# Kernel tuning notes

Hardware: AMD Instinct MI355X
Metric: run time of the kernel (lower is better)

## Reference

```python
import jax, jax.numpy as jnp
import numpy as np

K = 3
KK = K * K


def conv3x3(x, w, b):
    # x: [B,C,H,W], w: [O,C,3,3]
    y = jax.lax.conv_general_dilated(x, w, (1, 1), ((1, 1), (1, 1)),
                                     dimension_numbers=('NCHW', 'OIHW', 'NCHW'))
    return y + b[None, :, None, None]


def deform_conv(x, offset, w, b):
    # torchvision.ops.deform_conv2d, 3x3, pad=1, stride=1, no mask.
    B, C, H, W = x.shape
    off = offset.reshape(B, KK, 2, H, W)  # per kernel tap: (dy, dx)
    ky = jnp.repeat(jnp.arange(K, dtype=x.dtype) - 1, K)  # [9]
    kx = jnp.tile(jnp.arange(K, dtype=x.dtype) - 1, K)
    py = jnp.arange(H, dtype=x.dtype)[None, None, :, None] + ky[None, :, None, None] + off[:, :, 0]
    px = jnp.arange(W, dtype=x.dtype)[None, None, None, :] + kx[None, :, None, None] + off[:, :, 1]
    y0 = jnp.floor(py)
    x0 = jnp.floor(px)
    wy = (py - y0)[:, None]  # [B,1,9,H,W]
    wx = (px - x0)[:, None]
    y0i = y0.astype(jnp.int32)
    x0i = x0.astype(jnp.int32)
    xf = x.reshape(B, C, H * W)

    def corner(yi, xi):
        valid = ((yi >= 0) & (yi < H) & (xi >= 0) & (xi < W))
        idx = jnp.clip(yi, 0, H - 1) * W + jnp.clip(xi, 0, W - 1)  # [B,9,H,W]
        g = jax.vmap(lambda xb, ib: xb[:, ib.reshape(-1)])(xf, idx)  # [B,C,9*H*W]
        return g.reshape(B, C, KK, H, W) * valid[:, None].astype(x.dtype)

    val = (corner(y0i, x0i) * (1 - wy) * (1 - wx)
           + corner(y0i, x0i + 1) * (1 - wy) * wx
           + corner(y0i + 1, x0i) * wy * (1 - wx)
           + corner(y0i + 1, x0i + 1) * wy * wx)  # [B,C,9,H,W]
    out = jnp.einsum('bckhw,ock->bohw', val, w.reshape(w.shape[0], C, KK))
    return out + b[None, :, None, None]


def se_gate(x, w1, b1, w2, b2):
    # global avg pool -> 1x1 conv -> relu -> 1x1 conv -> sigmoid -> scale
    m = x.mean((2, 3))  # [B,C]
    h = jax.nn.relu(jnp.einsum('bc,rc->br', m, w1) + b1)
    g = jax.nn.sigmoid(jnp.einsum('br,cr->bc', h, w2) + b2)
    return x * g[:, :, None, None]


def resize_bilinear(x, oh, ow):
    # F.interpolate(mode='bilinear', align_corners=False)
    B, C, H, W = x.shape

    def coords(n_in, n_out):
        src = (jnp.arange(n_out, dtype=x.dtype) + 0.5) * (n_in / n_out) - 0.5
        src = jnp.clip(src, 0.0, n_in - 1)
        i0 = jnp.floor(src).astype(jnp.int32)
        i1 = jnp.minimum(i0 + 1, n_in - 1)
        return i0, i1, (src - i0).astype(x.dtype)

    y0, y1, wy = coords(H, oh)
    x = x[:, :, y0, :] * (1 - wy)[None, None, :, None] + x[:, :, y1, :] * wy[None, None, :, None]
    c0, c1, wc = coords(W, ow)
    x = x[:, :, :, c0] * (1 - wc)[None, None, None, :] + x[:, :, :, c1] * wc[None, None, None, :]
    return x


def setup_inputs() -> dict:
    key = jax.random.key(0)
    ks = jax.random.split(key, 12)
    B, C, H, W = 4, 64, 128, 128
    L, O, R = 4, 64, 4  # levels, out_channels, reduction=64//16
    d = {
        'x': jax.random.normal(ks[0], (B, C, H, W), jnp.float32),
        'off_w': jax.random.normal(ks[1], (L, 2 * KK, C, 3, 3), jnp.float32) * 0.01,
        'off_b': jax.random.normal(ks[2], (L, 2 * KK), jnp.float32) * 0.01,
        'dc_w': jax.random.normal(ks[3], (L, O, C, 3, 3), jnp.float32) * 0.05,
        'dc_b': jax.random.normal(ks[4], (L, O), jnp.float32) * 0.05,
        'se_w1': jax.random.normal(ks[5], (L, R, O), jnp.float32) * 0.1,
        'se_b1': jax.random.normal(ks[6], (L, R), jnp.float32) * 0.1,
        'se_w2': jax.random.normal(ks[7], (L, O, R), jnp.float32) * 0.1,
        'se_b2': jax.random.normal(ks[8], (L, O), jnp.float32) * 0.1,
        'fuse_w': jax.random.normal(ks[9], (O, L * O), jnp.float32) * 0.05,
        'fuse_b': jax.random.normal(ks[10], (O,), jnp.float32) * 0.05,
    }
    return d


def reference(x, off_w, off_b, dc_w, dc_b, se_w1, se_b1, se_w2, se_b2, fuse_w, fuse_b):
    B, _, H, W = x.shape
    L = off_w.shape[0]
    cur = x
    feats = []
    for i in range(L):
        if i > 0:
            cur = resize_bilinear(cur, cur.shape[2] // 2, cur.shape[3] // 2)
        off = conv3x3(cur, off_w[i], off_b[i])
        cur = deform_conv(cur, off, dc_w[i], dc_b[i])
        cur = se_gate(cur, se_w1[i], se_b1[i], se_w2[i], se_b2[i])
        feats.append(resize_bilinear(cur, H, W))
    for i in range(L - 2, -1, -1):
        feats[i] = feats[i] + feats[i + 1]
    fused = jnp.concatenate(feats, axis=1)  # [B, L*O, H, W]
    return jnp.einsum('bchw,oc->bohw', fused, fuse_w) + fuse_b[None, :, None, None]
```

## Files before the change

### kernel.cpp

```cpp
#include <hip/hip_runtime.h>
#include <hip/hip_bf16.h>
#include <math.h>


constexpr int Bn = 4;

typedef __attribute__((ext_vector_type(8))) short short8;
typedef __attribute__((ext_vector_type(4))) float f32x4;
typedef __attribute__((ext_vector_type(4))) unsigned uint4v;

static __device__ __forceinline__ short f2b(float f){
  union { float f; unsigned u; } v; v.f = f;
  unsigned r = v.u + 0x7fffu + ((v.u >> 16) & 1u);
  return (short)(r >> 16);
}
static __device__ __forceinline__ unsigned f2b2(float x, float y){
  union { __hip_bfloat162 h; unsigned u; } cv;
  cv.h = __float22bfloat162_rn(make_float2(x, y));
  return cv.u;
}
static __device__ __forceinline__ float blo(unsigned u){ return __uint_as_float(u << 16); }
static __device__ __forceinline__ float bhi(unsigned u){ return __uint_as_float(u & 0xffff0000u); }

constexpr size_t OFF_CUR   = 0;
constexpr size_t OFF_DC    = OFF_CUR  + 4194304;
constexpr size_t OFF_T0    = OFF_DC   + 4194304;
constexpr size_t OFF_T1    = OFF_T0   + 4194304;
constexpr size_t OFF_T2    = OFF_T1   + 1048576;
constexpr size_t OFF_T3    = OFF_T2   + 262144;
constexpr size_t OFF_WSUMT = OFF_T3   + 65536;
constexpr size_t OFF_DCWT  = OFF_WSUMT + 8192;
constexpr size_t OFF_OWT   = OFF_DCWT  + 73728;
constexpr size_t OFF_SUMS  = OFF_OWT   + 36864;

__global__ void prep_k(const float* __restrict__ dc_w, const float* __restrict__ off_w,
                       const float* __restrict__ fuse_w, float* __restrict__ ws){
  int i = blockIdx.x * 256 + threadIdx.x;
  short* dcwT  = (short*)(ws + OFF_DCWT);
  short* owT   = (short*)(ws + OFF_OWT);
  short* wsumT = (short*)(ws + OFF_WSUMT);
  if (i < 147456){
    int oc = i / 576, r = i % 576, k = r >> 6, c = r & 63;
    dcwT[i] = f2b(dc_w[(oc*64 + c)*9 + k]);
  } else if (i < 147456 + 73728){
    int t = i - 147456;
    int lm = t / 576, l = lm >> 5, m = lm & 31, r = t % 576, k = r >> 6, c = r & 63;
    owT[t] = (m < 18) ? f2b(off_w[((l*18 + m)*64 + c)*9 + k]) : (short)0;
  } else if (i < 147456 + 73728 + 16384){
    int t = i - (147456 + 73728);
    int l = t / 4096, r = t % 4096, o = r / 64, c = r % 64;
    float s = 0.f;
    for (int jl = 0; jl <= l; jl++) s += fuse_w[o*256 + jl*64 + c];
    wsumT[t] = f2b(s);
  } else if (i < 147456 + 73728 + 16384 + 65536){
    ws[OFF_SUMS + (i - (147456 + 73728 + 16384))] = 0.f;
  }
}

__global__ __launch_bounds__(256) void cvt_k(const float* __restrict__ x, unsigned* __restrict__ cur){
  __shared__ float t[64][65];
  int tile = blockIdx.x;
  int b = tile >> 8, p0 = (tile & 255) << 6;
  int tx = threadIdx.x & 63, ty = threadIdx.x >> 6;
  #pragma unroll
  for (int c = ty; c < 64; c += 4)
    t[c][tx] = x[(((size_t)(b << 6) + c) << 14) + p0 + tx];
  __syncthreads();
  int u = threadIdx.x & 31, pr = threadIdx.x >> 5;
  #pragma unroll
  for (int i = 0; i < 8; i++){
    int pp = pr + i*8;
    unsigned v = f2b2(t[2*u][pp], t[2*u + 1][pp]);
    cur[((size_t)(b << 14) + p0 + pp)*32 + u] = v;
  }
}

template<int H, int LVL>
__global__ __launch_bounds__(256, 6) void deform_k(
    const unsigned* __restrict__ cur, const float* __restrict__ ws_all,
    const float* __restrict__ off_bias, const float* __restrict__ dc_bias,
    float* __restrict__ dc, float* __restrict__ sums){
  constexpr int W = H, P = H * W;
  constexpr int PITCHB = 584 * 2;
  constexpr int TPR = W/4, TPB = P/16;
  __shared__ __align__(16) short valA[16][584];
  __shared__ float offsP[2][16][18];
  __shared__ float4 tapW[144];
  __shared__ int4   tapI[144];
  const short* owt = (const short*)(ws_all + OFF_OWT) + LVL * 32 * 576;
  const short* dcw = (const short*)(ws_all + OFF_DCWT) + (size_t)LVL * 64 * 576;
  const int tid = threadIdx.x;
  const int wave = tid >> 6, lane = tid & 63;
  const int c0 = lane & 15, quad = lane >> 4, q4 = quad * 4;
  const int half = lane >> 5, cc = lane & 31;
  const int b = blockIdx.x / TPB;
  const int rr = blockIdx.x % TPB;
  const int hrow = (rr / TPR) * 4, wcol = (rr % TPR) * 4;
  const char* curc = (const char*)(cur + (size_t)b * P * 32) + cc * 4;
  char* valc = (char*)valA + wave * (4 * PITCHB);

  #pragma unroll
  for (int i = 0; i < 18; i++){
    const int t0 = 2*i, t1 = t0 + 1;
    const int p0l = t0/9, k0 = t0%9, p1l = t1/9, k1 = t1%9;
    int yy0 = hrow + wave + k0/3 - 1, xx0 = wcol + p0l + k0%3 - 1;
    int yy1 = hrow + wave + k1/3 - 1, xx1 = wcol + p1l + k1%3 - 1;
    bool v0 = ((unsigned)yy0 < (unsigned)H) & ((unsigned)xx0 < (unsigned)W);
    bool v1 = ((unsigned)yy1 < (unsigned)H) & ((unsigned)xx1 < (unsigned)W);
    int  i0 = v0 ? (yy0*W + xx0) : 0,  i1 = v1 ? (yy1*W + xx1) : 0;
    int   idx = half ? i1 : i0;
    bool  vv  = half ? v1 : v0;
    unsigned uv = *(const unsigned*)(curc + (size_t)idx * 128);
    uv = vv ? uv : 0u;
    const int ob0 = p0l*PITCHB + k0*128, ob1 = p1l*PITCHB + k1*128;
    *(unsigned*)(valc + (half ? ob1 : ob0) + cc*4) = uv;
  }
  __syncthreads();

  {
    const int colw = wave & 1, kh = wave >> 1;
    f32x4 oacc = {0,0,0,0};
    #pragma unroll
    for (int kb = 0; kb < 9; kb++){
      int kk = kh*9 + kb;
      short8 a  = *(const short8*)&valA[c0][kk*32 + quad*8];
      short8 bf = *(const short8*)&owt[(colw*16 + c0)*576 + kk*32 + quad*8];
      oacc = __builtin_amdgcn_mfma_f32_16x16x32_bf16(a, bf, oacc, 0, 0, 0);
    }
    int comp = colw*16 + c0;
    if (comp < 18){
      #pragma unroll
      for (int r = 0; r < 4; r++) offsP[kh][q4 + r][comp] = oacc[r];
    }
  }
  __syncthreads();

  if (tid < 144){
    int p = tid / 9, k = tid % 9;
    int h = hrow + (p >> 2), w = wcol + (p & 3);
    float oy = offsP[0][p][2*k]     + offsP[1][p][2*k]     + off_bias[LVL*18 + 2*k];
    float ox = offsP[0][p][2*k + 1] + offsP[1][p][2*k + 1] + off_bias[LVL*18 + 2*k + 1];
    float py = (float)(h + k/3 - 1) + oy;
    float px = (float)(w + k%3 - 1) + ox;
    float y0f = floorf(py), x0f = floorf(px);
    float fy = py - y0f, fx = px - x0f;
    int y0 = (int)y0f, x0 = (int)x0f, y1 = y0 + 1, x1 = x0 + 1;
    bool vy0 = (y0 >= 0) & (y0 < H), vy1 = (y1 >= 0) & (y1 < H);
    bool vx0 = (x0 >= 0) & (x0 < W), vx1 = (x1 >= 0) & (x1 < W);
    int y0c = min(max(y0, 0), H-1), y1c = min(max(y1, 0), H-1);
    int x0c = min(max(x0, 0), W-1), x1c = min(max(x1, 0), W-1);
    float gy = 1.f - fy, gx = 1.f - fx;
    tapW[tid] = make_float4((vy0 & vx0) ? gy*gx : 0.f,
                            (vy0 & vx1) ? gy*fx : 0.f,
                            (vy1 & vx0) ? fy*gx : 0.f,
                            (vy1 & vx1) ? fy*fx : 0.f);
    tapI[tid] = make_int4((y0c*W + x0c) << 7, (y0c*W + x1c) << 7,
                          (y1c*W + x0c) << 7, (y1c*W + x1c) << 7);
  }
  __syncthreads();

  #pragma unroll
  for (int i = 0; i < 18; i++){
    int T = wave*36 + 2*i + half;
    float4 wv = tapW[T];
    int4   ti = tapI[T];
    unsigned u0 = *(const unsigned*)(curc + ti.x);
    unsigned u1 = *(const unsigned*)(curc + ti.y);
    unsigned u2 = *(const unsigned*)(curc + ti.z);
    unsigned u3 = *(const unsigned*)(curc + ti.w);
    float vx = wv.x*blo(u0) + wv.y*blo(u1) + wv.z*blo(u2) + wv.w*blo(u3);
    float vy = wv.x*bhi(u0) + wv.y*bhi(u1) + wv.z*bhi(u2) + wv.w*bhi(u3);
    unsigned pk = f2b2(vx, vy);
    const int t0 = 2*i, t1 = t0 + 1;
    const int ob0 = (t0/9)*PITCHB + (t0%9)*128, ob1 = (t1/9)*PITCHB + (t1%9)*128;
    *(unsigned*)(valc + (half ? ob1 : ob0) + cc*4) = pk;
  }
  __syncthreads();

  const int n = wave*16 + c0;
  float bt2 = dc_bias[LVL*64 + n];
  f32x4 d0 = {bt2, bt2, bt2, bt2}, d1 = {0,0,0,0};
  #pragma unroll
  for (int kb = 0; kb < 9; kb++){
    short8 a  = *(const short8*)&valA[c0][kb*32 + quad*8];
    short8 bf = *(const short8*)&dcw[n*576 + kb*32 + quad*8];
    d0 = __builtin_amdgcn_mfma_f32_16x16x32_bf16(a, bf, d0, 0, 0, 0);
  }
  #pragma unroll
  for (int kb = 9; kb < 18; kb++){
    short8 a  = *(const short8*)&valA[c0][kb*32 + quad*8];
    short8 bf = *(const short8*)&dcw[n*576 + kb*32 + quad*8];
    d1 = __builtin_amdgcn_mfma_f32_16x16x32_bf16(a, bf, d1, 0, 0, 0);
  }
  f32x4 acc;
  #pragma unroll
  for (int r = 0; r < 4; r++) acc[r] = d0[r] + d1[r];
  float* dcb = dc + ((size_t)b*P + (size_t)(hrow + quad)*W + wcol)*64;
  #pragma unroll
  for (int r = 0; r < 4; r++) dcb[r*64 + n] = acc[r];
  float s = acc[0] + acc[1] + acc[2] + acc[3];
  s += __shfl_xor(s, 16);
  s += __shfl_xor(s, 32);
  if (quad == 0) atomicAdd(&sums[(LVL*16 + (blockIdx.x & 15))*256 + (b << 6) + n], s);
}

template<int W, int LVL>
__global__ __launch_bounds__(256) void fuse_gd_k(
    const float* __restrict__ dcv, const float* __restrict__ sums,
    const float* __restrict__ se_w1, const float* __restrict__ se_b1,
    const float* __restrict__ se_w2, const float* __restrict__ se_b2,
    const float* __restrict__ ws_all, float* __restrict__ tmp, unsigned* __restrict__ curn){
  constexpr int P = W * W;
  constexpr bool POOL = (LVL < 3);
  constexpr float invP = 1.f / (float)P;
  __shared__ __align__(16) float fS[64][68];
  __shared__ __align__(16) float gsh[64];
  const short* wsl = (const short*)(ws_all + OFF_WSUMT) + LVL * 4096;
  const int tid = threadIdx.x, wave = tid >> 6, lane = tid & 63;
  const int c0 = lane & 15, quad = lane >> 4, q4 = quad * 4;
  int b, rp = 0, cs = 0;
  if (POOL){
    constexpr int tilesPerB = P / 64, tilesPerRow = W / 32;
    b = blockIdx.x / tilesPerB;
    int r = blockIdx.x % tilesPerB;
    rp = r / tilesPerRow; cs = r % tilesPerRow;
  } else {
    b = (blockIdx.x * 64) / P;
  }

  {
    int sg = tid >> 6, c = tid & 63;
    float part = 0.f;
    #pragma unroll
    for (int s = 0; s < 4; s++) part += sums[(LVL*16 + sg*4 + s)*256 + (b << 6) + c];
    fS[sg][c] = part;
    __syncthreads();
    if (tid < 64){
      int r = tid & 3, j = tid >> 2;
      float hp = 0.f;
      #pragma unroll
      for (int q = 0; q < 4; q++){
        int cq = j*4 + q;
        float m = (fS[0][cq] + fS[1][cq] + fS[2][cq] + fS[3][cq]) * invP;
        hp += m * se_w1[(LVL*4 + r)*64 + cq];
      }
      hp += __shfl_xor(hp, 4);  hp += __shfl_xor(hp, 8);
      hp += __shfl_xor(hp, 16); hp += __shfl_xor(hp, 32);
      float hr = fmaxf(hp + se_b1[LVL*4 + r], 0.f);
      float a = se_b2[LVL*64 + tid];
      #pragma unroll
      for (int r2 = 0; r2 < 4; r2++)
        a += __shfl(hr, r2) * se_w2[(LVL*64 + tid)*4 + r2];
      gsh[tid] = 1.f / (1.f + expf(-a));
    }
    __syncthreads();
  }

  float4 g4 = *(const float4*)&gsh[c0*4];
  #pragma unroll
  for (int i = 0; i < 4; i++){
    int lp = wave*16 + (lane >> 4) + i*4;
    size_t gpix = POOL ? ((size_t)b*P + (size_t)(2*rp + (lp >> 5))*W + cs*32 + (lp & 31))
                       : ((size_t)blockIdx.x*64 + lp);
    float4 d = *(const float4*)&dcv[gpix*64 + c0*4];
    float4 v = make_float4(d.x*g4.x, d.y*g4.y, d.z*g4.z, d.w*g4.w);
    *(float4*)&fS[lp][c0*4] = v;
  }
  __syncthreads();
  f32x4 acc[4] = {{0,0,0,0},{0,0,0,0},{0,0,0,0},{0,0,0,0}};
  #pragma unroll
  for (int kb = 0; kb < 2; kb++){
    float4 lo = *(const float4*)&fS[wave*16 + c0][kb*32 + quad*8];
    float4 hi = *(const float4*)&fS[wave*16 + c0][kb*32 + quad*8 + 4];
    uint4v ua = {f2b2(lo.x, lo.y), f2b2(lo.z, lo.w), f2b2(hi.x, hi.y), f2b2(hi.z, hi.w)};
    short8 a = __builtin_bit_cast(short8, ua);
    #pragma unroll
    for (int t = 0; t < 4; t++){
      short8 bf = *(const short8*)&wsl[(t*16 + c0)*64 + kb*32 + quad*8];
      acc[t] = __builtin_amdgcn_mfma_f32_16x16x32_bf16(a, bf, acc[t], 0, 0, 0);
    }
  }
  #pragma unroll
  for (int t = 0; t < 4; t++){
    int n = t*16 + c0;
    size_t plane = ((size_t)(b << 6) + n) * P;
    size_t pix = POOL ? ((size_t)(2*rp + (wave >> 1))*W + cs*32 + (wave & 1)*16 + q4)
                      : ((size_t)(blockIdx.x*64) - (size_t)b*P + wave*16 + q4);
    *(f32x4*)&tmp[plane + pix] = acc[t];
  }
  if constexpr (POOL){
    int j = tid >> 4, uu = tid & 15;
    float4 p0 = *(const float4*)&fS[2*j][uu*4];
    float4 p1 = *(const float4*)&fS[2*j + 1][uu*4];
    float4 p2 = *(const float4*)&fS[32 + 2*j][uu*4];
    float4 p3 = *(const float4*)&fS[33 + 2*j][uu*4];
    float4 av = make_float4(0.25f*(p0.x + p1.x + p2.x + p3.x),
                            0.25f*(p0.y + p1.y + p2.y + p3.y),
                            0.25f*(p0.z + p1.z + p2.z + p3.z),
                            0.25f*(p0.w + p1.w + p2.w + p3.w));
    uint2 pv = make_uint2(f2b2(av.x, av.y), f2b2(av.z, av.w));
    *(uint2*)&curn[((size_t)b*(P/4) + (size_t)rp*(W/2) + cs*16 + j)*32 + uu*2] = pv;
  }
}

__global__ void final_k(const float* __restrict__ ws_all, const float* __restrict__ fuse_bias,
                        float* __restrict__ out){
  int i = blockIdx.x * 256 + threadIdx.x;
  int w = i & 127, h = (i >> 7) & 127, o = (i >> 14) & 63, b = i >> 20;
  float acc = fuse_bias[o] + ws_all[OFF_T0 + (((size_t)(b << 6) + o) << 14) + (h << 7) + w];
  const float* tarr[3] = {ws_all + OFF_T1, ws_all + OFF_T2, ws_all + OFF_T3};
  #pragma unroll
  for (int li = 0; li < 3; li++){
    int l = li + 1, Hl = 128 >> l;
    float scale = 1.0f / (float)(1 << l);
    float sy = fminf(fmaxf((h + 0.5f)*scale - 0.5f, 0.f), (float)(Hl - 1));
    float sx = fminf(fmaxf((w + 0.5f)*scale - 0.5f, 0.f), (float)(Hl - 1));
    int y0 = (int)sy, x0 = (int)sx;
    float fy = sy - y0, fx = sx - x0;
    int y1 = min(y0 + 1, Hl - 1), x1 = min(x0 + 1, Hl - 1);
    const float* tb = tarr[li] + (size_t)((b << 6) + o) * Hl * Hl;
    float v00 = tb[y0*Hl + x0], v01 = tb[y0*Hl + x1];
    float v10 = tb[y1*Hl + x0], v11 = tb[y1*Hl + x1];
    acc += (1.f-fy)*((1.f-fx)*v00 + fx*v01) + fy*((1.f-fx)*v10 + fx*v11);
  }
  out[i] = acc;
}

extern "C" void kernel_launch(void* const* d_in, const int* in_sizes, int n_in,
                              void* d_out, int out_size, void* d_ws, size_t ws_size,
                              hipStream_t stream){
  (void)in_sizes; (void)n_in; (void)out_size; (void)ws_size;
  const float* x      = (const float*)d_in[0];
  const float* off_w  = (const float*)d_in[1];
  const float* off_b  = (const float*)d_in[2];
  const float* dc_w   = (const float*)d_in[3];
  const float* dc_b   = (const float*)d_in[4];
  const float* se_w1  = (const float*)d_in[5];
  const float* se_b1  = (const float*)d_in[6];
  const float* se_w2  = (const float*)d_in[7];
  const float* se_b2  = (const float*)d_in[8];
  const float* fuse_w = (const float*)d_in[9];
  const float* fuse_b = (const float*)d_in[10];
  float* out = (float*)d_out;
  float* ws = (float*)d_ws;
  unsigned* cur = (unsigned*)(ws + OFF_CUR);
  float* dc   = ws + OFF_DC;
  float* tmp[4] = {ws + OFF_T0, ws + OFF_T1, ws + OFF_T2, ws + OFF_T3};
  float* sums = ws + OFF_SUMS;

  prep_k<<<(303104 + 255)/256, 256, 0, stream>>>(dc_w, off_w, fuse_w, ws);
  cvt_k<<<1024, 256, 0, stream>>>(x, cur);

  deform_k<128,0><<<4096, 256, 0, stream>>>(cur, ws, off_b, dc_b, dc, sums);
  fuse_gd_k<128,0><<<1024, 256, 0, stream>>>(dc, sums, se_w1, se_b1, se_w2, se_b2, ws, tmp[0], cur);
  deform_k<64,1><<<1024, 256, 0, stream>>>(cur, ws, off_b, dc_b, dc, sums);
  fuse_gd_k<64,1><<<256, 256, 0, stream>>>(dc, sums, se_w1, se_b1, se_w2, se_b2, ws, tmp[1], cur);
  deform_k<32,2><<<256, 256, 0, stream>>>(cur, ws, off_b, dc_b, dc, sums);
  fuse_gd_k<32,2><<<64, 256, 0, stream>>>(dc, sums, se_w1, se_b1, se_w2, se_b2, ws, tmp[2], cur);
  deform_k<16,3><<<64, 256, 0, stream>>>(cur, ws, off_b, dc_b, dc, sums);
  fuse_gd_k<16,3><<<16, 256, 0, stream>>>(dc, sums, se_w1, se_b1, se_w2, se_b2, ws, tmp[3], nullptr);

  final_k<<<16384, 256, 0, stream>>>(ws, fuse_b, out);
}
```

Before: 234.4 us.

## Stage 8x8 input window in LDS for deform taps and merge prep kernels

```diff
diff --git a/kernel.cpp b/kernel.cpp
--- a/kernel.cpp
+++ b/kernel.cpp
@@ -33,9 +33,30 @@
 constexpr size_t OFF_OWT   = OFF_DCWT  + 73728;
 constexpr size_t OFF_SUMS  = OFF_OWT   + 36864;
 
-__global__ void prep_k(const float* __restrict__ dc_w, const float* __restrict__ off_w,
-                       const float* __restrict__ fuse_w, float* __restrict__ ws){
-  int i = blockIdx.x * 256 + threadIdx.x;
+__global__ __launch_bounds__(256) void init_k(const float* __restrict__ x,
+                                              const float* __restrict__ dc_w,
+                                              const float* __restrict__ off_w,
+                                              const float* __restrict__ fuse_w,
+                                              float* __restrict__ ws, unsigned* __restrict__ cur){
+  if (blockIdx.x < 1024){
+    __shared__ float t[64][65];
+    int tile = blockIdx.x;
+    int b = tile >> 8, p0 = (tile & 255) << 6;
+    int tx = threadIdx.x & 63, ty = threadIdx.x >> 6;
+    #pragma unroll
+    for (int c = ty; c < 64; c += 4)
+      t[c][tx] = x[(((size_t)(b << 6) + c) << 14) + p0 + tx];
+    __syncthreads();
+    int u = threadIdx.x & 31, pr = threadIdx.x >> 5;
+    #pragma unroll
+    for (int i = 0; i < 8; i++){
+      int pp = pr + i*8;
+      unsigned v = f2b2(t[2*u][pp], t[2*u + 1][pp]);
+      cur[((size_t)(b << 14) + p0 + pp)*32 + u] = v;
+    }
+    return;
+  }
+  int i = (blockIdx.x - 1024) * 256 + threadIdx.x;
   short* dcwT  = (short*)(ws + OFF_DCWT);
   short* owT   = (short*)(ws + OFF_OWT);
   short* wsumT = (short*)(ws + OFF_WSUMT);
@@ -57,26 +78,8 @@
   }
 }
 
-__global__ __launch_bounds__(256) void cvt_k(const float* __restrict__ x, unsigned* __restrict__ cur){
-  __shared__ float t[64][65];
-  int tile = blockIdx.x;
-  int b = tile >> 8, p0 = (tile & 255) << 6;
-  int tx = threadIdx.x & 63, ty = threadIdx.x >> 6;
-  #pragma unroll
-  for (int c = ty; c < 64; c += 4)
-    t[c][tx] = x[(((size_t)(b << 6) + c) << 14) + p0 + tx];
-  __syncthreads();
-  int u = threadIdx.x & 31, pr = threadIdx.x >> 5;
-  #pragma unroll
-  for (int i = 0; i < 8; i++){
-    int pp = pr + i*8;
-    unsigned v = f2b2(t[2*u][pp], t[2*u + 1][pp]);
-    cur[((size_t)(b << 14) + p0 + pp)*32 + u] = v;
-  }
-}
-
 template<int H, int LVL>
-__global__ __launch_bounds__(256, 6) void deform_k(
+__global__ __launch_bounds__(256, 4) void deform_k(
     const unsigned* __restrict__ cur, const float* __restrict__ ws_all,
     const float* __restrict__ off_bias, const float* __restrict__ dc_bias,
     float* __restrict__ dc, float* __restrict__ sums){
@@ -84,9 +87,11 @@
   constexpr int PITCHB = 584 * 2;
   constexpr int TPR = W/4, TPB = P/16;
   __shared__ __align__(16) short valA[16][584];
+  __shared__ __align__(16) unsigned win[8*8*32];
   __shared__ float offsP[2][16][18];
   __shared__ float4 tapW[144];
   __shared__ int4   tapI[144];
+  __shared__ int    tapF[144];
   const short* owt = (const short*)(ws_all + OFF_OWT) + LVL * 32 * 576;
   const short* dcw = (const short*)(ws_all + OFF_DCWT) + (size_t)LVL * 64 * 576;
   const int tid = threadIdx.x;
@@ -96,22 +101,35 @@
   const int b = blockIdx.x / TPB;
   const int rr = blockIdx.x % TPB;
   const int hrow = (rr / TPR) * 4, wcol = (rr % TPR) * 4;
-  const char* curc = (const char*)(cur + (size_t)b * P * 32) + cc * 4;
+  const unsigned* curb = cur + (size_t)b * P * 32;
+  const char* curc = (const char*)curb + cc * 4;
   char* valc = (char*)valA + wave * (4 * PITCHB);
+
+  {
+    int wy = tid >> 5, l32 = tid & 31;
+    int y = hrow - 2 + wy;
+    #pragma unroll
+    for (int hh = 0; hh < 2; hh++){
+      int u = l32*8 + hh*4;
+      int px = u >> 5, ccc = u & 31;
+      int xx = wcol - 2 + px;
+      uint4v v = {0,0,0,0};
+      if (((unsigned)y < (unsigned)H) & ((unsigned)xx < (unsigned)W))
+        v = *(const uint4v*)(curb + ((size_t)(y*W + xx))*32 + ccc);
+      *(uint4v*)&win[(wy*8 + px)*32 + ccc] = v;
+    }
+  }
+  __syncthreads();
 
   #pragma unroll
   for (int i = 0; i < 18; i++){
     const int t0 = 2*i, t1 = t0 + 1;
     const int p0l = t0/9, k0 = t0%9, p1l = t1/9, k1 = t1%9;
-    int yy0 = hrow + wave + k0/3 - 1, xx0 = wcol + p0l + k0%3 - 1;
-    int yy1 = hrow + wave + k1/3 - 1, xx1 = wcol + p1l + k1%3 - 1;
-    bool v0 = ((unsigned)yy0 < (unsigned)H) & ((unsigned)xx0 < (unsigned)W);
-    bool v1 = ((unsigned)yy1 < (unsigned)H) & ((unsigned)xx1 < (unsigned)W);
-    int  i0 = v0 ? (yy0*W + xx0) : 0,  i1 = v1 ? (yy1*W + xx1) : 0;
-    int   idx = half ? i1 : i0;
-    bool  vv  = half ? v1 : v0;
-    unsigned uv = *(const unsigned*)(curc + (size_t)idx * 128);
-    uv = vv ? uv : 0u;
+    const int wy0 = k0/3 + 1, wx0 = p0l + k0%3 + 1;
+    const int wy1 = k1/3 + 1, wx1 = p1l + k1%3 + 1;
+    int wy = (half ? wy1 : wy0) + wave;
+    int wx = half ? wx1 : wx0;
+    unsigned uv = win[((wy << 3) + wx)*32 + cc];
     const int ob0 = p0l*PITCHB + k0*128, ob1 = p1l*PITCHB + k1*128;
     *(unsigned*)(valc + (half ? ob1 : ob0) + cc*4) = uv;
   }
@@ -154,20 +172,38 @@
                             (vy0 & vx1) ? gy*fx : 0.f,
                             (vy1 & vx0) ? fy*gx : 0.f,
                             (vy1 & vx1) ? fy*fx : 0.f);
-    tapI[tid] = make_int4((y0c*W + x0c) << 7, (y0c*W + x1c) << 7,
-                          (y1c*W + x0c) << 7, (y1c*W + x1c) << 7);
-  }
-  __syncthreads();
-
+    bool ok = (y0c >= hrow-2) & (y1c <= hrow+5) & (x0c >= wcol-2) & (x1c <= wcol+5);
+    tapF[tid] = ok ? 1 : 0;
+    if (ok){
+      int ry0 = y0c - hrow + 2, ry1 = y1c - hrow + 2;
+      int rx0 = x0c - wcol + 2, rx1 = x1c - wcol + 2;
+      tapI[tid] = make_int4(((ry0<<3) + rx0) << 7, ((ry0<<3) + rx1) << 7,
+                            ((ry1<<3) + rx0) << 7, ((ry1<<3) + rx1) << 7);
+    } else {
+      tapI[tid] = make_int4((y0c*W + x0c) << 7, (y0c*W + x1c) << 7,
+                            (y1c*W + x0c) << 7, (y1c*W + x1c) << 7);
+    }
+  }
+  __syncthreads();
+
+  const char* winc = (const char*)win + cc * 4;
   #pragma unroll
   for (int i = 0; i < 18; i++){
     int T = wave*36 + 2*i + half;
     float4 wv = tapW[T];
     int4   ti = tapI[T];
-    unsigned u0 = *(const unsigned*)(curc + ti.x);
-    unsigned u1 = *(const unsigned*)(curc + ti.y);
-    unsigned u2 = *(const unsigned*)(curc + ti.z);
-    unsigned u3 = *(const unsigned*)(curc + ti.w);
+    unsigned u0, u1, u2, u3;
+    if (tapF[T]){
+      u0 = *(const unsigned*)(winc + ti.x);
+      u1 = *(const unsigned*)(winc + ti.y);
+      u2 = *(const unsigned*)(winc + ti.z);
+      u3 = *(const unsigned*)(winc + ti.w);
+    } else {
+      u0 = *(const unsigned*)(curc + ti.x);
+      u1 = *(const unsigned*)(curc + ti.y);
+      u2 = *(const unsigned*)(curc + ti.z);
+      u3 = *(const unsigned*)(curc + ti.w);
+    }
     float vx = wv.x*blo(u0) + wv.y*blo(u1) + wv.z*blo(u2) + wv.w*blo(u3);
     float vy = wv.x*bhi(u0) + wv.y*bhi(u1) + wv.z*bhi(u2) + wv.w*bhi(u3);
     unsigned pk = f2b2(vx, vy);
@@ -348,8 +384,7 @@
   float* tmp[4] = {ws + OFF_T0, ws + OFF_T1, ws + OFF_T2, ws + OFF_T3};
   float* sums = ws + OFF_SUMS;
 
-  prep_k<<<(303104 + 255)/256, 256, 0, stream>>>(dc_w, off_w, fuse_w, ws);
-  cvt_k<<<1024, 256, 0, stream>>>(x, cur);
+  init_k<<<1024 + (303104 + 255)/256, 256, 0, stream>>>(x, dc_w, off_w, fuse_w, ws, cur);
 
   deform_k<128,0><<<4096, 256, 0, stream>>>(cur, ws, off_b, dc_b, dc, sums);
   fuse_gd_k<128,0><<<1024, 256, 0, stream>>>(dc, sums, se_w1, se_b1, se_w2, se_b2, ws, tmp[0], cur);
```

New measurement: 235.2 us. No clear change (+0.4%).
